# Optimization experiments

Measured on AMD Instinct MI355X. Metric: run time of the kernel, lower is better.

The kernel has to match this reference:

```python
import jax, jax.numpy as jnp
import numpy as np

ALPHA = 0.2  # leaky_relu negative slope


def setup_inputs() -> dict:
    key = jax.random.key(0)
    ks = jax.random.split(key, 6)
    N, E, F_IN, F_OUT, E_DIM = 50000, 800000, 256, 256, 64
    h = jax.random.normal(ks[0], (N, F_IN), dtype=jnp.float32)
    e_feat = jax.random.normal(ks[1], (E, E_DIM), dtype=jnp.float32)
    W = jax.random.normal(ks[2], (F_OUT, F_IN), dtype=jnp.float32) * (1.0 / np.sqrt(F_IN))
    A = jax.random.normal(ks[3], (1, 2 * F_OUT + E_DIM), dtype=jnp.float32) * 0.05
    src = jax.random.randint(ks[4], (E,), 0, N, dtype=jnp.int32)
    dst = jax.random.randint(ks[5], (E,), 0, N, dtype=jnp.int32)
    return {"h": h, "e_feat": e_feat, "W": W, "A": A, "src": src, "dst": dst}


def reference(h, e_feat, W, A, src, dst):
    N = h.shape[0]
    F_OUT = W.shape[0]
    # equation (1): node projection
    z = h @ W.T  # [N, F_OUT]
    z_src = z[src]  # [E, F_OUT]
    z_dst = z[dst]  # [E, F_OUT]
    # equation (2): per-edge attention logit = attn_fc([z_src, z_dst, e_feat])
    # split A to avoid materializing the [E, 2F+De] concat
    a_src, a_dst, a_e = A[0, :F_OUT], A[0, F_OUT:2 * F_OUT], A[0, 2 * F_OUT:]
    logits = z_src @ a_src + z_dst @ a_dst + e_feat @ a_e  # [E]
    e = jax.nn.leaky_relu(logits, ALPHA)
    # equations (3)&(4): segment-softmax over incoming edges per destination
    m = jax.ops.segment_max(e, dst, num_segments=N)  # [N]
    ex = jnp.exp(e - m[dst])
    denom = jax.ops.segment_sum(ex, dst, num_segments=N)  # [N]
    alpha = ex / denom[dst]  # [E]
    h_out = jax.ops.segment_sum(alpha[:, None] * z_src, dst, num_segments=N)
    return h_out
```

## Files before the change

kernel.cpp:

```cpp
#include <hip/hip_runtime.h>
#include <hip/hip_bf16.h>

#define FDIM 256
#define EDIM 64
#define LEAKY 0.2f

#define BM 128
#define BN 256
#define BK 32

typedef __attribute__((ext_vector_type(8))) short bfrag;
typedef __attribute__((ext_vector_type(4))) float f4acc;

__device__ __forceinline__ unsigned f2bf(float x){
    unsigned u = __float_as_uint(x);
    return (u + 0x7FFFu + ((u >> 16) & 1u)) >> 16;
}
__device__ __forceinline__ float bf2f(unsigned b){
    return __uint_as_float(b << 16);
}
__device__ __forceinline__ unsigned pack_hi(float x, float y, float& hx, float& hy){
    unsigned bx = f2bf(x), by = f2bf(y);
    hx = bf2f(bx); hy = bf2f(by);
    return bx | (by << 16);
}
__device__ __forceinline__ unsigned pack_lo(float rx, float ry){
    return f2bf(rx) | (f2bf(ry) << 16);
}

__global__ void k_wconv(const float* __restrict__ W, unsigned short* __restrict__ W16){
    int i = (blockIdx.x*256 + threadIdx.x) * 4;
    float4 v = *(const float4*)&W[i];
    uint2 o;
    o.x = f2bf(v.x) | (f2bf(v.y) << 16);
    o.y = f2bf(v.z) | (f2bf(v.w) << 16);
    *(uint2*)&W16[i] = o;
}

__global__ __launch_bounds__(256, 2) void k_gemm(const float* __restrict__ h,
                                                 const unsigned short* __restrict__ W16,
                                                 const float* __restrict__ A,
                                                 unsigned short* __restrict__ z16,
                                                 float* __restrict__ s_src,
                                                 float* __restrict__ s_dst, int M){
    __shared__ uint4 smA[BM*8];
    __shared__ uint4 smB[BN*8];
    __shared__ float sred[2][2][BM];

    int tid = threadIdx.x;
    int m0 = blockIdx.x * BM;

    int wid  = tid >> 6;
    int lane = tid & 63;
    int wm = (wid >> 1) * 64;
    int wn = (wid & 1) * 128;
    int l15 = lane & 15;
    int l4  = lane >> 4;

    f4acc acc[4][8];
    #pragma unroll
    for (int i = 0; i < 4; ++i)
        #pragma unroll
        for (int j = 0; j < 8; ++j)
            acc[i][j] = (f4acc)(0.f);

    for (int kc = 0; kc < FDIM; kc += BK){
        #pragma unroll
        for (int q = 0; q < 6; ++q){
            int p = tid + q*256;
            if (p < 512){
                int row = p >> 2, k8 = p & 3;
                int gr = m0 + row;
                float4 v0, v1;
                if (gr < M){
                    const float* g = &h[(size_t)gr*FDIM + kc + k8*8];
                    v0 = *(const float4*)g; v1 = *(const float4*)(g + 4);
                } else {
                    v0 = make_float4(0.f,0.f,0.f,0.f); v1 = v0;
                }
                uint4 hi, lo; float hx, hy;
                hi.x = pack_hi(v0.x, v0.y, hx, hy);
                lo.x = pack_lo(v0.x - hx, v0.y - hy);
                hi.y = pack_hi(v0.z, v0.w, hx, hy);
                lo.y = pack_lo(v0.z - hx, v0.w - hy);
                hi.z = pack_hi(v1.x, v1.y, hx, hy);
                lo.z = pack_lo(v1.x - hx, v1.y - hy);
                hi.w = pack_hi(v1.z, v1.w, hx, hy);
                lo.w = pack_lo(v1.z - hx, v1.w - hy);
                int sh = k8 ^ (row & 7);
                smA[row*8 + sh]       = hi;
                smA[row*8 + (sh ^ 4)] = lo;
            } else {
                int pb = p - 512;
                int row = pb >> 2, k8 = pb & 3;
                uint4 v = *(const uint4*)&W16[(size_t)row*FDIM + kc + k8*8];
                smB[row*8 + (k8 ^ (row & 7))] = v;
            }
        }
        __syncthreads();

        bfrag ah[4], al[4];
        #pragma unroll
        for (int mf = 0; mf < 4; ++mf){
            int row = wm + mf*16 + l15;
            int sh = l4 ^ (row & 7);
            ah[mf] = *(const bfrag*)&smA[row*8 + sh];
            al[mf] = *(const bfrag*)&smA[row*8 + (sh ^ 4)];
        }
        #pragma unroll
        for (int nf = 0; nf < 8; ++nf){
            int row = wn + nf*16 + l15;
            bfrag bh = *(const bfrag*)&smB[row*8 + (l4 ^ (row & 7))];
            #pragma unroll
            for (int mf = 0; mf < 4; ++mf){
                acc[mf][nf] = __builtin_amdgcn_mfma_f32_16x16x32_bf16(ah[mf], bh, acc[mf][nf], 0, 0, 0);
                acc[mf][nf] = __builtin_amdgcn_mfma_f32_16x16x32_bf16(al[mf], bh, acc[mf][nf], 0, 0, 0);
            }
        }
        __syncthreads();
    }

    #pragma unroll
    for (int mf = 0; mf < 4; ++mf){
        #pragma unroll
        for (int nf = 0; nf < 8; ++nf){
            int gcol = wn + nf*16 + l15;
            #pragma unroll
            for (int r = 0; r < 4; ++r){
                int grow = m0 + wm + mf*16 + l4*4 + r;
                if (grow < M)
                    z16[(size_t)grow*FDIM + gcol] = (unsigned short)f2bf(acc[mf][nf][r]);
            }
        }
    }

    float aS[8], aD[8];
    #pragma unroll
    for (int nf = 0; nf < 8; ++nf){
        int gcol = wn + nf*16 + l15;
        aS[nf] = A[gcol];
        aD[nf] = A[FDIM + gcol];
    }
    #pragma unroll
    for (int mf = 0; mf < 4; ++mf){
        #pragma unroll
        for (int r = 0; r < 4; ++r){
            float ps = 0.f, pd = 0.f;
            #pragma unroll
            for (int nf = 0; nf < 8; ++nf){
                ps += acc[mf][nf][r] * aS[nf];
                pd += acc[mf][nf][r] * aD[nf];
            }
            #pragma unroll
            for (int o = 1; o < 16; o <<= 1){
                ps += __shfl_xor(ps, o);
                pd += __shfl_xor(pd, o);
            }
            if (l15 == 0){
                int row = wm + mf*16 + l4*4 + r;
                sred[wid & 1][0][row] = ps;
                sred[wid & 1][1][row] = pd;
            }
        }
    }
    __syncthreads();
    if (tid < BM){
        int grow = m0 + tid;
        if (grow < M){
            s_src[grow] = sred[0][0][tid] + sred[1][0][tid];
            s_dst[grow] = sred[0][1][tid] + sred[1][1][tid];
        }
    }
}

__global__ void k_count(const int* __restrict__ dst, int* __restrict__ counts, int E){
    int e = blockIdx.x*256 + threadIdx.x;
    if (e < E) atomicAdd(&counts[dst[e]], 1);
}

__global__ void k_chunk_sums(const int* __restrict__ counts, int* __restrict__ bsums, int N){
    __shared__ int sh[256];
    int base = blockIdx.x*1024;
    int s = 0;
    for (int i = threadIdx.x; i < 1024; i += 256){
        int idx = base + i;
        s += (idx < N) ? counts[idx] : 0;
    }
    sh[threadIdx.x] = s; __syncthreads();
    for (int o = 128; o > 0; o >>= 1){
        if (threadIdx.x < o) sh[threadIdx.x] += sh[threadIdx.x + o];
        __syncthreads();
    }
    if (threadIdx.x == 0) bsums[blockIdx.x] = sh[0];
}

__global__ void k_scan_small(int* __restrict__ b, int nb){
    __shared__ int sh[1024];
    int tid = threadIdx.x;
    int v = (tid < nb) ? b[tid] : 0;
    sh[tid] = v; __syncthreads();
    int acc = v;
    for (int o = 1; o < 1024; o <<= 1){
        int t = (tid >= o) ? sh[tid - o] : 0;
        __syncthreads();
        acc += t; sh[tid] = acc;
        __syncthreads();
    }
    if (tid < nb) b[tid] = acc - v;
}

__global__ void k_scan_chunks(int* __restrict__ counts, int* __restrict__ cursor,
                              const int* __restrict__ bsums, int N, int E){
    __shared__ int sh[256];
    int tid = threadIdx.x;
    int base = blockIdx.x*1024 + tid*4;
    int v[4]; int s = 0;
    #pragma unroll
    for (int l = 0; l < 4; l++){
        int idx = base + l;
        v[l] = (idx < N) ? counts[idx] : 0;
        s += v[l];
    }
    sh[tid] = s; __syncthreads();
    int acc = s;
    for (int o = 1; o < 256; o <<= 1){
        int t = (tid >= o) ? sh[tid - o] : 0;
        __syncthreads();
        acc += t; sh[tid] = acc;
        __syncthreads();
    }
    int excl = acc - s + bsums[blockIdx.x];
    #pragma unroll
    for (int l = 0; l < 4; l++){
        int idx = base + l;
        if (idx < N){ counts[idx] = excl; cursor[idx] = excl; }
        excl += v[l];
    }
    if (blockIdx.x == 0 && tid == 0) counts[N] = E;
}

__global__ void k_edge(const float* __restrict__ ef, const float* __restrict__ A,
                       const float* __restrict__ s_src, const float* __restrict__ s_dst,
                       const int* __restrict__ src, const int* __restrict__ dst,
                       int* __restrict__ cursor, int2* __restrict__ epair, int E){
    int gt = blockIdx.x*256 + threadIdx.x;
    int e = gt >> 4, l4 = gt & 15;
    if (e >= E) return;
    float4 f  = *(const float4*)&ef[(size_t)e*EDIM + l4*4];
    float4 ae = *(const float4*)&A[2*FDIM + l4*4];
    float v = f.x*ae.x + f.y*ae.y + f.z*ae.z + f.w*ae.w;
    v += __shfl_xor(v, 8); v += __shfl_xor(v, 4);
    v += __shfl_xor(v, 2); v += __shfl_xor(v, 1);
    if (l4 == 0){
        int d = dst[e];
        float lg = v + s_src[src[e]] + s_dst[d];
        lg = lg > 0.f ? lg : LEAKY*lg;
        int p = atomicAdd(&cursor[d], 1);
        int2 pr; pr.x = src[e]; pr.y = __float_as_int(lg);
        epair[p] = pr;
    }
}

__global__ __launch_bounds__(256) void k_out(const unsigned short* __restrict__ z16,
                                             const int* __restrict__ offsets,
                                             const int2* __restrict__ epair,
                                             float* __restrict__ out, int N){
    int n = blockIdx.x*4 + (threadIdx.x >> 6);
    int lane = threadIdx.x & 63;
    if (n >= N) return;
    int i0 = offsets[n], i1 = offsets[n+1];

    float mlane = -3.402823466e38f;
    for (int i = i0 + lane; i < i1; i += 64)
        mlane = fmaxf(mlane, __int_as_float(epair[i].y));
    float mx = mlane;
    #pragma unroll
    for (int o = 32; o > 0; o >>= 1)
        mx = fmaxf(mx, __shfl_xor(mx, o));

    float4 a[4];
    a[0] = make_float4(0,0,0,0); a[1] = a[0]; a[2] = a[0]; a[3] = a[0];
    float dw = 0.f;
    const unsigned short* zb = z16 + lane*4;

    for (int base = i0; base < i1; base += 64){
        int cnt = min(64, i1 - base);
        int2 pe = make_int2(0, 0);
        float w = 0.f;
        if (lane < cnt){
            pe = epair[base + lane];
            w = __expf(__int_as_float(pe.y) - mx);
        }
        dw += w;
        int j = 0;
        for (; j + 7 < cnt; j += 8){
            float wj[8]; int sj[8]; uint2 rj[8];
            #pragma unroll
            for (int q = 0; q < 8; ++q){
                wj[q] = __shfl(w, j + q);
                sj[q] = __shfl(pe.x, j + q);
            }
            #pragma unroll
            for (int q = 0; q < 8; ++q)
                rj[q] = *(const uint2*)&zb[(size_t)sj[q]*FDIM];
            #pragma unroll
            for (int q = 0; q < 8; ++q){
                a[q & 3].x += wj[q]*bf2f(rj[q].x & 0xffffu);
                a[q & 3].y += wj[q]*bf2f(rj[q].x >> 16);
                a[q & 3].z += wj[q]*bf2f(rj[q].y & 0xffffu);
                a[q & 3].w += wj[q]*bf2f(rj[q].y >> 16);
            }
        }
        for (; j < cnt; ++j){
            float wq = __shfl(w, j);
            int   sq = __shfl(pe.x, j);
            uint2 r0 = *(const uint2*)&zb[(size_t)sq*FDIM];
            a[0].x += wq*bf2f(r0.x & 0xffffu);
            a[0].y += wq*bf2f(r0.x >> 16);
            a[0].z += wq*bf2f(r0.y & 0xffffu);
            a[0].w += wq*bf2f(r0.y >> 16);
        }
    }

    #pragma unroll
    for (int o = 32; o > 0; o >>= 1)
        dw += __shfl_xor(dw, o);

    float inv = (i1 > i0) ? 1.f / dw : 0.f;
    float4 res;
    res.x = ((a[0].x + a[1].x) + (a[2].x + a[3].x)) * inv;
    res.y = ((a[0].y + a[1].y) + (a[2].y + a[3].y)) * inv;
    res.z = ((a[0].z + a[1].z) + (a[2].z + a[3].z)) * inv;
    res.w = ((a[0].w + a[1].w) + (a[2].w + a[3].w)) * inv;
    *(float4*)&out[(size_t)n*FDIM + lane*4] = res;
}

extern "C" void kernel_launch(void* const* d_in, const int* in_sizes, int n_in,
                              void* d_out, int out_size, void* d_ws, size_t ws_size,
                              hipStream_t stream){
    const float* h  = (const float*)d_in[0];
    const float* ef = (const float*)d_in[1];
    const float* W  = (const float*)d_in[2];
    const float* A  = (const float*)d_in[3];
    const int*  src = (const int*)d_in[4];
    const int*  dst = (const int*)d_in[5];
    float* out = (float*)d_out;
    int N = in_sizes[0] / FDIM;
    int E = in_sizes[4];

    char* ws = (char*)d_ws;
    size_t off = 0;
    auto alloc = [&](size_t nbytes)->char*{
        char* p = ws + off;
        off = (off + nbytes + 255) & ~(size_t)255;
        return p;
    };
    unsigned short* z16 = (unsigned short*)alloc((size_t)N*FDIM*2);
    unsigned short* W16 = (unsigned short*)alloc((size_t)FDIM*FDIM*2);
    float* s_src  = (float*)alloc((size_t)N*4);
    float* s_dst  = (float*)alloc((size_t)N*4);
    int*   counts = (int*)alloc((size_t)(N+1)*4);
    int*   cursor = (int*)alloc((size_t)N*4);
    int2*  epair  = (int2*)alloc((size_t)E*8);
    int*   bsums  = (int*)alloc(1024*4);

    int nb = (N + 1023)/1024;

    hipMemsetAsync(counts, 0, (size_t)(N+1)*4, stream);
    hipLaunchKernelGGL(k_wconv, dim3(64), dim3(256), 0, stream, W, W16);
    hipLaunchKernelGGL(k_gemm, dim3((N+BM-1)/BM), dim3(256), 0, stream,
                       h, W16, A, z16, s_src, s_dst, N);
    hipLaunchKernelGGL(k_count, dim3((E+255)/256), dim3(256), 0, stream,
                       dst, counts, E);
    hipLaunchKernelGGL(k_chunk_sums, dim3(nb), dim3(256), 0, stream,
                       counts, bsums, N);
    hipLaunchKernelGGL(k_scan_small, dim3(1), dim3(1024), 0, stream,
                       bsums, nb);
    hipLaunchKernelGGL(k_scan_chunks, dim3(nb), dim3(256), 0, stream,
                       counts, cursor, bsums, N, E);
    hipLaunchKernelGGL(k_edge, dim3((E+15)/16), dim3(256), 0, stream,
                       ef, A, s_src, s_dst, src, dst, cursor, epair, E);
    hipLaunchKernelGGL(k_out, dim3((N+3)/4), dim3(256), 0, stream,
                       z16, counts, epair, out, N);
}
```

Before: 230.1 us.

## Fuse prep kernels, collapse scan into one grid-barrier kernel, retile GEMM

Merges the W-to-bf16 conversion and the destination-count atomics into one prep kernel. Replaces the three-kernel prefix scan with a single 64-block kernel that synchronises through two global atomic barriers, cutting launch count and gaps between launches. Also shrinks the GEMM M-tile from 128 to 64, with each wave covering a 64-column strip, and raises launch bounds to 3 blocks per CU for more occupancy. The costs are more redundant W tile loads per output row and a spin barrier that assumes all 64 scan blocks are resident at once.

```diff
diff --git a/kernel.cpp b/kernel.cpp
--- a/kernel.cpp
+++ b/kernel.cpp
@@ -5,9 +5,10 @@
 #define EDIM 64
 #define LEAKY 0.2f
 
-#define BM 128
-#define BN 256
+#define BM 64
 #define BK 32
+
+#define SCAN_BLOCKS 64
 
 typedef __attribute__((ext_vector_type(8))) short bfrag;
 typedef __attribute__((ext_vector_type(4))) float f4acc;
@@ -28,87 +29,102 @@
     return f2bf(rx) | (f2bf(ry) << 16);
 }
 
-__global__ void k_wconv(const float* __restrict__ W, unsigned short* __restrict__ W16){
-    int i = (blockIdx.x*256 + threadIdx.x) * 4;
-    float4 v = *(const float4*)&W[i];
-    uint2 o;
-    o.x = f2bf(v.x) | (f2bf(v.y) << 16);
-    o.y = f2bf(v.z) | (f2bf(v.w) << 16);
-    *(uint2*)&W16[i] = o;
-}
-
-__global__ __launch_bounds__(256, 2) void k_gemm(const float* __restrict__ h,
+__device__ __forceinline__ void gbar(int* bar, int idx, int nb){
+    __syncthreads();
+    if (threadIdx.x == 0){
+        __threadfence();
+        atomicAdd(&bar[idx], 1);
+        while (__hip_atomic_load(&bar[idx], __ATOMIC_ACQUIRE, __HIP_MEMORY_SCOPE_AGENT) < nb){}
+        __threadfence();
+    }
+    __syncthreads();
+}
+
+__global__ void k_prep(const float* __restrict__ W, unsigned short* __restrict__ W16,
+                       const int* __restrict__ dst, int* __restrict__ counts,
+                       int* __restrict__ bar, int E){
+    int gt = blockIdx.x*256 + threadIdx.x;
+    if (gt == 0){ bar[0] = 0; bar[1] = 0; }
+    if (gt < (FDIM*FDIM)/4){
+        int i = gt*4;
+        float4 v = *(const float4*)&W[i];
+        uint2 o;
+        o.x = f2bf(v.x) | (f2bf(v.y) << 16);
+        o.y = f2bf(v.z) | (f2bf(v.w) << 16);
+        *(uint2*)&W16[i] = o;
+    }
+    if (gt < E) atomicAdd(&counts[dst[gt]], 1);
+}
+
+__global__ __launch_bounds__(256, 3) void k_gemm(const float* __restrict__ h,
                                                  const unsigned short* __restrict__ W16,
                                                  const float* __restrict__ A,
                                                  unsigned short* __restrict__ z16,
                                                  float* __restrict__ s_src,
                                                  float* __restrict__ s_dst, int M){
     __shared__ uint4 smA[BM*8];
-    __shared__ uint4 smB[BN*8];
-    __shared__ float sred[2][2][BM];
+    __shared__ uint4 smB[FDIM*8];
+    __shared__ float sred[4][2][BM];
 
     int tid = threadIdx.x;
     int m0 = blockIdx.x * BM;
 
     int wid  = tid >> 6;
     int lane = tid & 63;
-    int wm = (wid >> 1) * 64;
-    int wn = (wid & 1) * 128;
+    int wn = wid * 64;
     int l15 = lane & 15;
     int l4  = lane >> 4;
 
-    f4acc acc[4][8];
+    f4acc acc[4][4];
     #pragma unroll
     for (int i = 0; i < 4; ++i)
         #pragma unroll
-        for (int j = 0; j < 8; ++j)
+        for (int j = 0; j < 4; ++j)
             acc[i][j] = (f4acc)(0.f);
 
     for (int kc = 0; kc < FDIM; kc += BK){
-        #pragma unroll
-        for (int q = 0; q < 6; ++q){
+        {
+            int row = tid >> 2, k8 = tid & 3;
+            int gr = m0 + row;
+            float4 v0, v1;
+            if (gr < M){
+                const float* g = &h[(size_t)gr*FDIM + kc + k8*8];
+                v0 = *(const float4*)g; v1 = *(const float4*)(g + 4);
+            } else {
+                v0 = make_float4(0.f,0.f,0.f,0.f); v1 = v0;
+            }
+            uint4 hi, lo; float hx, hy;
+            hi.x = pack_hi(v0.x, v0.y, hx, hy);
+            lo.x = pack_lo(v0.x - hx, v0.y - hy);
+            hi.y = pack_hi(v0.z, v0.w, hx, hy);
+            lo.y = pack_lo(v0.z - hx, v0.w - hy);
+            hi.z = pack_hi(v1.x, v1.y, hx, hy);
+            lo.z = pack_lo(v1.x - hx, v1.y - hy);
+            hi.w = pack_hi(v1.z, v1.w, hx, hy);
+            lo.w = pack_lo(v1.z - hx, v1.w - hy);
+            int sh = k8 ^ (row & 7);
+            smA[row*8 + sh]       = hi;
+            smA[row*8 + (sh ^ 4)] = lo;
+        }
+        #pragma unroll
+        for (int q = 0; q < 4; ++q){
             int p = tid + q*256;
-            if (p < 512){
-                int row = p >> 2, k8 = p & 3;
-                int gr = m0 + row;
-                float4 v0, v1;
-                if (gr < M){
-                    const float* g = &h[(size_t)gr*FDIM + kc + k8*8];
-                    v0 = *(const float4*)g; v1 = *(const float4*)(g + 4);
-                } else {
-                    v0 = make_float4(0.f,0.f,0.f,0.f); v1 = v0;
-                }
-                uint4 hi, lo; float hx, hy;
-                hi.x = pack_hi(v0.x, v0.y, hx, hy);
-                lo.x = pack_lo(v0.x - hx, v0.y - hy);
-                hi.y = pack_hi(v0.z, v0.w, hx, hy);
-                lo.y = pack_lo(v0.z - hx, v0.w - hy);
-                hi.z = pack_hi(v1.x, v1.y, hx, hy);
-                lo.z = pack_lo(v1.x - hx, v1.y - hy);
-                hi.w = pack_hi(v1.z, v1.w, hx, hy);
-                lo.w = pack_lo(v1.z - hx, v1.w - hy);
-                int sh = k8 ^ (row & 7);
-                smA[row*8 + sh]       = hi;
-                smA[row*8 + (sh ^ 4)] = lo;
-            } else {
-                int pb = p - 512;
-                int row = pb >> 2, k8 = pb & 3;
-                uint4 v = *(const uint4*)&W16[(size_t)row*FDIM + kc + k8*8];
-                smB[row*8 + (k8 ^ (row & 7))] = v;
-            }
+            int row = p >> 2, k8 = p & 3;
+            uint4 v = *(const uint4*)&W16[(size_t)row*FDIM + kc + k8*8];
+            smB[row*8 + (k8 ^ (row & 7))] = v;
         }
         __syncthreads();
 
         bfrag ah[4], al[4];
         #pragma unroll
         for (int mf = 0; mf < 4; ++mf){
-            int row = wm + mf*16 + l15;
+            int row = mf*16 + l15;
             int sh = l4 ^ (row & 7);
             ah[mf] = *(const bfrag*)&smA[row*8 + sh];
             al[mf] = *(const bfrag*)&smA[row*8 + (sh ^ 4)];
         }
         #pragma unroll
-        for (int nf = 0; nf < 8; ++nf){
+        for (int nf = 0; nf < 4; ++nf){
             int row = wn + nf*16 + l15;
             bfrag bh = *(const bfrag*)&smB[row*8 + (l4 ^ (row & 7))];
             #pragma unroll
@@ -123,20 +139,20 @@
     #pragma unroll
     for (int mf = 0; mf < 4; ++mf){
         #pragma unroll
-        for (int nf = 0; nf < 8; ++nf){
+        for (int nf = 0; nf < 4; ++nf){
             int gcol = wn + nf*16 + l15;
             #pragma unroll
             for (int r = 0; r < 4; ++r){
-                int grow = m0 + wm + mf*16 + l4*4 + r;
+                int grow = m0 + mf*16 + l4*4 + r;
                 if (grow < M)
                     z16[(size_t)grow*FDIM + gcol] = (unsigned short)f2bf(acc[mf][nf][r]);
             }
         }
     }
 
-    float aS[8], aD[8];
-    #pragma unroll
-    for (int nf = 0; nf < 8; ++nf){
+    float aS[4], aD[4];
+    #pragma unroll
+    for (int nf = 0; nf < 4; ++nf){
         int gcol = wn + nf*16 + l15;
         aS[nf] = A[gcol];
         aD[nf] = A[FDIM + gcol];
@@ -147,7 +163,7 @@
         for (int r = 0; r < 4; ++r){
             float ps = 0.f, pd = 0.f;
             #pragma unroll
-            for (int nf = 0; nf < 8; ++nf){
+            for (int nf = 0; nf < 4; ++nf){
                 ps += acc[mf][nf][r] * aS[nf];
                 pd += acc[mf][nf][r] * aD[nf];
             }
@@ -157,9 +173,9 @@
                 pd += __shfl_xor(pd, o);
             }
             if (l15 == 0){
-                int row = wm + mf*16 + l4*4 + r;
-                sred[wid & 1][0][row] = ps;
-                sred[wid & 1][1][row] = pd;
+                int row = mf*16 + l4*4 + r;
+                sred[wid][0][row] = ps;
+                sred[wid][1][row] = pd;
             }
         }
     }
@@ -167,73 +183,67 @@
     if (tid < BM){
         int grow = m0 + tid;
         if (grow < M){
-            s_src[grow] = sred[0][0][tid] + sred[1][0][tid];
-            s_dst[grow] = sred[0][1][tid] + sred[1][1][tid];
-        }
-    }
-}
-
-__global__ void k_count(const int* __restrict__ dst, int* __restrict__ counts, int E){
-    int e = blockIdx.x*256 + threadIdx.x;
-    if (e < E) atomicAdd(&counts[dst[e]], 1);
-}
-
-__global__ void k_chunk_sums(const int* __restrict__ counts, int* __restrict__ bsums, int N){
-    __shared__ int sh[256];
-    int base = blockIdx.x*1024;
-    int s = 0;
-    for (int i = threadIdx.x; i < 1024; i += 256){
-        int idx = base + i;
-        s += (idx < N) ? counts[idx] : 0;
-    }
-    sh[threadIdx.x] = s; __syncthreads();
-    for (int o = 128; o > 0; o >>= 1){
-        if (threadIdx.x < o) sh[threadIdx.x] += sh[threadIdx.x + o];
-        __syncthreads();
-    }
-    if (threadIdx.x == 0) bsums[blockIdx.x] = sh[0];
-}
-
-__global__ void k_scan_small(int* __restrict__ b, int nb){
-    __shared__ int sh[1024];
-    int tid = threadIdx.x;
-    int v = (tid < nb) ? b[tid] : 0;
-    sh[tid] = v; __syncthreads();
-    int acc = v;
-    for (int o = 1; o < 1024; o <<= 1){
-        int t = (tid >= o) ? sh[tid - o] : 0;
-        __syncthreads();
-        acc += t; sh[tid] = acc;
-        __syncthreads();
-    }
-    if (tid < nb) b[tid] = acc - v;
-}
-
-__global__ void k_scan_chunks(int* __restrict__ counts, int* __restrict__ cursor,
-                              const int* __restrict__ bsums, int N, int E){
+            s_src[grow] = (sred[0][0][tid] + sred[1][0][tid]) + (sred[2][0][tid] + sred[3][0][tid]);
+            s_dst[grow] = (sred[0][1][tid] + sred[1][1][tid]) + (sred[2][1][tid] + sred[3][1][tid]);
+        }
+    }
+}
+
+__global__ __launch_bounds__(256) void k_scan(int* __restrict__ counts, int* __restrict__ cursor,
+                                              int* __restrict__ bsums, int* __restrict__ bar,
+                                              int N, int E){
     __shared__ int sh[256];
     int tid = threadIdx.x;
-    int base = blockIdx.x*1024 + tid*4;
-    int v[4]; int s = 0;
+    int chunk = (N + SCAN_BLOCKS - 1) / SCAN_BLOCKS;
+    int c0 = blockIdx.x * chunk;
+    int lim = min(c0 + chunk, N);
+
+    int s = 0;
+    for (int i = c0 + tid; i < lim; i += 256) s += counts[i];
+    sh[tid] = s; __syncthreads();
+    for (int o = 128; o > 0; o >>= 1){
+        if (tid < o) sh[tid] += sh[tid + o];
+        __syncthreads();
+    }
+    if (tid == 0) bsums[blockIdx.x] = sh[0];
+
+    gbar(bar, 0, SCAN_BLOCKS);
+
+    if (blockIdx.x == 0 && tid < 64){
+        int v = bsums[tid];
+        int orig = v;
+        #pragma unroll
+        for (int o = 1; o < 64; o <<= 1){
+            int t = __shfl_up(v, o);
+            if (tid >= o) v += t;
+        }
+        bsums[tid] = v - orig;
+    }
+
+    gbar(bar, 1, SCAN_BLOCKS);
+
+    int base = c0 + tid*4;
+    int v[4]; int ts = 0;
     #pragma unroll
     for (int l = 0; l < 4; l++){
         int idx = base + l;
-        v[l] = (idx < N) ? counts[idx] : 0;
-        s += v[l];
-    }
-    sh[tid] = s; __syncthreads();
-    int acc = s;
+        v[l] = (idx < lim) ? counts[idx] : 0;
+        ts += v[l];
+    }
+    __syncthreads();
+    sh[tid] = ts; __syncthreads();
+    int acc = ts;
     for (int o = 1; o < 256; o <<= 1){
         int t = (tid >= o) ? sh[tid - o] : 0;
         __syncthreads();
         acc += t; sh[tid] = acc;
         __syncthreads();
     }
-    int excl = acc - s + bsums[blockIdx.x];
+    int excl = acc - ts + bsums[blockIdx.x];
     #pragma unroll
     for (int l = 0; l < 4; l++){
         int idx = base + l;
-        if (idx < N){ counts[idx] = excl; cursor[idx] = excl; }
+        if (idx < lim){ counts[idx] = excl; cursor[idx] = excl; }
         excl += v[l];
     }
     if (blockIdx.x == 0 && tid == 0) counts[N] = E;
@@ -362,22 +372,16 @@
     int*   counts = (int*)alloc((size_t)(N+1)*4);
     int*   cursor = (int*)alloc((size_t)N*4);
     int2*  epair  = (int2*)alloc((size_t)E*8);
-    int*   bsums  = (int*)alloc(1024*4);
-
-    int nb = (N + 1023)/1024;
+    int*   bsums  = (int*)alloc(SCAN_BLOCKS*4);
+    int*   bar    = (int*)alloc(2*4);
 
     hipMemsetAsync(counts, 0, (size_t)(N+1)*4, stream);
-    hipLaunchKernelGGL(k_wconv, dim3(64), dim3(256), 0, stream, W, W16);
+    hipLaunchKernelGGL(k_prep, dim3((E+255)/256), dim3(256), 0, stream,
+                       W, W16, dst, counts, bar, E);
     hipLaunchKernelGGL(k_gemm, dim3((N+BM-1)/BM), dim3(256), 0, stream,
                        h, W16, A, z16, s_src, s_dst, N);
-    hipLaunchKernelGGL(k_count, dim3((E+255)/256), dim3(256), 0, stream,
-                       dst, counts, E);
-    hipLaunchKernelGGL(k_chunk_sums, dim3(nb), dim3(256), 0, stream,
-                       counts, bsums, N);
-    hipLaunchKernelGGL(k_scan_small, dim3(1), dim3(1024), 0, stream,
-                       bsums, nb);
-    hipLaunchKernelGGL(k_scan_chunks, dim3(nb), dim3(256), 0, stream,
-                       counts, cursor, bsums, N, E);
+    hipLaunchKernelGGL(k_scan, dim3(SCAN_BLOCKS), dim3(256), 0, stream,
+                       counts, cursor, bsums, bar, N, E);
     hipLaunchKernelGGL(k_edge, dim3((E+15)/16), dim3(256), 0, stream,
                        ef, A, s_src, s_dst, src, dst, cursor, epair, E);
     hipLaunchKernelGGL(k_out, dim3((N+3)/4), dim3(256), 0, stream,
```

After: 238.8 us. +3.8%, slower.
